# Optimization experiments

Measured on AMD Instinct MI355X. Metric: run time of the kernel, lower is better.

## Reference

```python
import jax, jax.numpy as jnp
import numpy as np

B, C, L = 4, 512, 2048
CI = 512          # inter_channels (must equal num_heads*head_dim)
H, D = 8, 64      # num_heads, head_dim = C // H
EPS = 1e-5        # BatchNorm1d eps


def setup_inputs() -> dict:
    key = jax.random.key(0)
    ks = jax.random.split(key, 9)
    s_in = 1.0 / np.sqrt(C)
    s_ci = 1.0 / np.sqrt(CI)
    return {
        "x": jax.random.normal(ks[0], (B, C, L), dtype=jnp.float32),
        "g_w": jax.random.uniform(ks[1], (CI, C), jnp.float32, -s_in, s_in),
        "g_b": jax.random.uniform(ks[2], (CI,), jnp.float32, -s_in, s_in),
        "theta_w": jax.random.uniform(ks[3], (CI, C), jnp.float32, -s_in, s_in),
        "theta_b": jax.random.uniform(ks[4], (CI,), jnp.float32, -s_in, s_in),
        "phi_w": jax.random.uniform(ks[5], (CI, C), jnp.float32, -s_in, s_in),
        "phi_b": jax.random.uniform(ks[6], (CI,), jnp.float32, -s_in, s_in),
        "w_w": jax.random.uniform(ks[7], (C, CI), jnp.float32, -s_ci, s_ci),
        "w_b": jax.random.uniform(ks[8], (C,), jnp.float32, -s_ci, s_ci),
        # BN affine params (torch inits them to 0, which zeroes the output;
        # use random values so the reference output / grads are non-trivial)
        "bn_gamma": jax.random.normal(jax.random.fold_in(key, 10), (C,), jnp.float32),
        "bn_beta": jax.random.normal(jax.random.fold_in(key, 11), (C,), jnp.float32),
    }


def _conv1x1(w, b, x):
    # x: [B, Cin, L], w: [Cout, Cin] -> [B, Cout, L]
    return jnp.einsum("oc,bcl->bol", w, x) + b[None, :, None]


def reference(x, g_w, g_b, theta_w, theta_b, phi_w, phi_b, w_w, w_b, bn_gamma, bn_beta):
    b, _, l = x.shape
    # 1x1 conv projections, split into heads: [B, H, D, L]
    g_x = _conv1x1(g_w, g_b, x).reshape(b, H, D, l).transpose(0, 1, 3, 2)      # [B,H,L,D]
    theta_x = _conv1x1(theta_w, theta_b, x).reshape(b, H, D, l).transpose(0, 1, 3, 2)  # [B,H,L,D]
    phi_x = _conv1x1(phi_w, phi_b, x).reshape(b, H, D, l)                       # [B,H,D,L]

    scale = 1.0 / jnp.sqrt(jnp.asarray(D, dtype=x.dtype))
    scores = jnp.einsum("bhqd,bhdk->bhqk", theta_x, phi_x) * scale  # [B,H,L,L]
    attn = jax.nn.softmax(scores, axis=-1)
    y = jnp.einsum("bhqk,bhkd->bhqd", attn, g_x)                    # [B,H,L,D]
    y = y.transpose(0, 1, 3, 2).reshape(b, CI, l)                   # [B,CI,L]

    # W: 1x1 conv + BatchNorm1d (training mode, biased batch stats)
    wy = _conv1x1(w_w, w_b, y)                                      # [B,C,L]
    mean = jnp.mean(wy, axis=(0, 2), keepdims=True)
    var = jnp.mean((wy - mean) ** 2, axis=(0, 2), keepdims=True)
    wy_hat = (wy - mean) * jax.lax.rsqrt(var + EPS)
    return wy_hat * bn_gamma[None, :, None] + bn_beta[None, :, None]
```

## Files before the change

kernel.cpp:

```cpp
#include <hip/hip_runtime.h>

constexpr int Bn = 4, Cn = 512, Ln = 2048, CIn = 512, Hn = 8, Dn = 64;
constexpr int COn = 3 * CIn;

typedef unsigned short u16;
typedef unsigned int u32;
typedef __attribute__((ext_vector_type(8))) short bfrag;
typedef __attribute__((ext_vector_type(4))) float facc;

#define SCF 0.180336879f

__device__ __forceinline__ facc mfma16(bfrag a, bfrag b, facc c) {
  return __builtin_amdgcn_mfma_f32_16x16x32_bf16(a, b, c, 0, 0, 0);
}

__device__ __forceinline__ void async16(const void* g, void* l) {
  __builtin_amdgcn_global_load_lds((const __attribute__((address_space(1))) void*)g,
                                   (__attribute__((address_space(3))) void*)l, 16, 0, 0);
}

__device__ __forceinline__ u16 f2bf(float x) {
  union { float f; u32 u; } v; v.f = x;
  u32 r = v.u + 0x7FFFu + ((v.u >> 16) & 1u);
  return (u16)(r >> 16);
}

__device__ __forceinline__ u16 f2bf_fast(float x) {
  union { float f; u32 u; } v; v.f = x;
  return (u16)((v.u + 0x8000u) >> 16);
}

__device__ __forceinline__ u32 pkbf(float lof, float hif) {
  union { float f; u32 u; } a, b; a.f = lof; b.f = hif;
  return __builtin_amdgcn_perm(b.u + 0x8000u, a.u + 0x8000u, 0x07060302u);
}

__device__ __forceinline__ float bflo(u32 u) { return __uint_as_float(u << 16); }
__device__ __forceinline__ float bfhi(u32 u) { return __uint_as_float(u & 0xFFFF0000u); }

__device__ __forceinline__ bfrag fr8(const u16* base, int row, int gi) {
  return *(const bfrag*)&base[row * 64 + ((gi ^ (row & 7)) * 8)];
}

__global__ void k_misc(const float* __restrict__ x, const float* __restrict__ gw,
                       const float* __restrict__ tw, const float* __restrict__ pw,
                       const float* __restrict__ ww, u16* __restrict__ xT,
                       u16* __restrict__ Wcat, u16* __restrict__ Ww,
                       float* __restrict__ stats) {
  int b = blockIdx.z;
  if (b == 4) {
    int i = (blockIdx.y * 64 + blockIdx.x) * 256 + threadIdx.x;
    if (i < CIn * Cn) {
      Wcat[i]                = f2bf(tw[i] * SCF);
      Wcat[CIn * Cn + i]     = f2bf(pw[i]);
      Wcat[2 * CIn * Cn + i] = f2bf(gw[i]);
      Ww[i]                  = f2bf(ww[i]);
    }
    if (i < 2 * Cn) stats[i] = 0.f;
    return;
  }
  __shared__ float tile[32][33];
  int l0 = blockIdx.x * 32, c0 = blockIdx.y * 32;
  int tx = threadIdx.x & 31, ty = threadIdx.x >> 5;
  const float* xb = x + (size_t)b * Cn * Ln;
  for (int k = 0; k < 4; k++)
    tile[ty + k * 8][tx] = xb[(size_t)(c0 + ty + k * 8) * Ln + l0 + tx];
  __syncthreads();
  u16* xtb = xT + (size_t)b * Ln * Cn;
  int cc = (threadIdx.x & 15) * 2, r0 = threadIdx.x >> 4;
  for (int k = 0; k < 2; k++) {
    int ll = r0 + k * 16;
    u32 pk = pkbf(tile[cc][ll], tile[cc + 1][ll]);
    *(u32*)&xtb[(size_t)(l0 + ll) * Cn + c0 + cc] = pk;
  }
}

__device__ __forceinline__ void stage128x32(const u16* g, int K, int k0, u16* lds,
                                            int w, int l) {
  int gsw = ((l & 3) ^ ((l >> 3) & 3)) * 8;
  for (int jj = 0; jj < 2; jj++) {
    int j = w * 2 + jj;
    const u16* ga = g + (size_t)(j * 16 + (l >> 2)) * K + k0 + gsw;
    async16(ga, (char*)lds + j * 1024 + l * 16);
  }
}

template <int SWAP>
__device__ __forceinline__ void gemm_core(const u16* A, const u16* Bt, int K,
                                          u16* As, u16* Bs, facc acc[4][4],
                                          int w, int l) {
  int quad = l >> 4, lo = l & 15;
  int mw = (w >> 1) * 64, nw = (w & 1) * 64;
  int rsw = (lo >> 1) & 3;
  for (int k0 = 0; k0 < K; k0 += 32) {
    stage128x32(A, K, k0, As, w, l);
    stage128x32(Bt, K, k0, Bs, w, l);
    __syncthreads();
    bfrag af[4], bfv[4];
    for (int mi = 0; mi < 4; mi++)
      af[mi] = *(const bfrag*)&As[(mw + mi * 16 + lo) * 32 + ((quad ^ rsw) * 8)];
    for (int ni = 0; ni < 4; ni++)
      bfv[ni] = *(const bfrag*)&Bs[(nw + ni * 16 + lo) * 32 + ((quad ^ rsw) * 8)];
    for (int mi = 0; mi < 4; mi++)
      for (int ni = 0; ni < 4; ni++)
        acc[mi][ni] = SWAP ? mfma16(bfv[ni], af[mi], acc[mi][ni])
                           : mfma16(af[mi], bfv[ni], acc[mi][ni]);
    __syncthreads();
  }
}

__device__ __forceinline__ void gemm_core64(const u16* A, const u16* Bt, int K,
                                            u16* As, u16* Bs, facc acc[2][4],
                                            int w, int l) {
  int quad = l >> 4, lo = l & 15;
  int mw = (w >> 1) * 32, nw = (w & 1) * 64;
  int rsw = (lo >> 1) & 3;
  int gsw = ((l & 3) ^ ((l >> 3) & 3)) * 8;
  for (int k0 = 0; k0 < K; k0 += 32) {
    async16(A + (size_t)(w * 16 + (l >> 2)) * K + k0 + gsw, (char*)As + w * 1024 + l * 16);
    stage128x32(Bt, K, k0, Bs, w, l);
    __syncthreads();
    bfrag af[2], bfv[4];
    for (int mi = 0; mi < 2; mi++)
      af[mi] = *(const bfrag*)&As[(mw + mi * 16 + lo) * 32 + ((quad ^ rsw) * 8)];
    for (int ni = 0; ni < 4; ni++)
      bfv[ni] = *(const bfrag*)&Bs[(nw + ni * 16 + lo) * 32 + ((quad ^ rsw) * 8)];
    for (int mi = 0; mi < 2; mi++)
      for (int ni = 0; ni < 4; ni++)
        acc[mi][ni] = mfma16(af[mi], bfv[ni], acc[mi][ni]);
    __syncthreads();
  }
}

__global__ __launch_bounds__(256) void k_proj(
    const u16* __restrict__ Wcat, const u16* __restrict__ xT,
    const float* __restrict__ tb, const float* __restrict__ pb,
    const float* __restrict__ gb, u16* __restrict__ Q, u16* __restrict__ Kb,
    u16* __restrict__ Vt) {
  __shared__ __align__(16) u16 As[128 * 32];
  __shared__ __align__(16) u16 Bs[128 * 32];
  int w = threadIdx.x >> 6, l = threadIdx.x & 63;
  int quad = l >> 4, lo = l & 15;
  int m0 = blockIdx.y * 128, n0 = blockIdx.x * 128, b = blockIdx.z;
  int chunk = m0 >> 9;
  facc acc[4][4] = {};
  const u16* Ap = Wcat + (size_t)m0 * Cn;
  const u16* Bp = xT + ((size_t)b * Ln + n0) * Cn;
  int mw = (w >> 1) * 64, nw = (w & 1) * 64;
  if (chunk < 2) {
    gemm_core<0>(Ap, Bp, Cn, As, Bs, acc, w, l);
    const float* bias = (chunk == 0) ? tb : pb;
    float bs = (chunk == 0) ? SCF : 1.0f;
    for (int mi = 0; mi < 4; mi++) {
      int mo = (m0 + mw + mi * 16) & 511;
      int hh = mo >> 6;
      int db = (mo & 63) + quad * 4;
      int bi = mo + quad * 4;
      u16* dst0 = ((chunk == 0) ? Q : Kb) + (size_t)(b * Hn + hh) * Ln * 64 + db;
      float b0 = bias[bi] * bs, b1 = bias[bi + 1] * bs;
      float b2 = bias[bi + 2] * bs, b3 = bias[bi + 3] * bs;
      for (int ni = 0; ni < 4; ni++) {
        int lcol = n0 + nw + ni * 16 + lo;
        facc a = acc[mi][ni];
        uint2 pk;
        pk.x = pkbf(a[0] + b0, a[1] + b1);
        pk.y = pkbf(a[2] + b2, a[3] + b3);
        *(uint2*)(dst0 + (size_t)lcol * 64) = pk;
      }
    }
  } else {
    gemm_core<1>(Ap, Bp, Cn, As, Bs, acc, w, l);
    for (int mi = 0; mi < 4; mi++) {
      int ch = (m0 + mw + mi * 16 + lo) & 511;
      int hh = ch >> 6, d = ch & 63;
      float bias = gb[ch];
      u16* dst0 = Vt + ((size_t)(b * Hn + hh) * Dn + d) * Ln;
      for (int ni = 0; ni < 4; ni++) {
        int l0 = n0 + nw + ni * 16 + quad * 4;
        facc a = acc[mi][ni];
        uint2 pk;
        pk.x = pkbf(a[0] + bias, a[1] + bias);
        pk.y = pkbf(a[2] + bias, a[3] + bias);
        *(uint2*)(dst0 + l0) = pk;
      }
    }
  }
}

__global__ __launch_bounds__(256, 2) void k_attn(
    const u16* __restrict__ Q, const u16* __restrict__ Kb,
    const u16* __restrict__ Vt, u16* __restrict__ Opart,
    float* __restrict__ lpart) {
  __shared__ __align__(16) u16 lds[24576];
  u16* Ks = lds;
  u16* Vs = lds + 8192;
  u16* QPs = lds + 16384;
  int w = threadIdx.x >> 6, l = threadIdx.x & 63;
  int quad = l >> 4, lo = l & 15;
  int q0 = blockIdx.x * 128, b = blockIdx.z;
  int h = blockIdx.y / 3, split = blockIdx.y - h * 3;
  int ts = split * 11;
  int nt = (split == 2) ? 10 : 11;
  size_t bh = (size_t)b * Hn + h;
  const u16* Qg = Q + bh * Ln * 64;
  const u16* Kg = Kb + bh * Ln * 64 + (size_t)ts * 4096;
  const u16* Vg = Vt + bh * (size_t)Dn * Ln + ts * 64;

  int rin = l >> 3;
  int gg = ((l & 7) ^ rin) * 8;

  for (int jj = 0; jj < 4; jj++) {
    int j = w * 4 + jj;
    async16(Qg + (size_t)(q0 + j * 8 + rin) * 64 + gg, (char*)QPs + j * 1024 + l * 16);
  }
  for (int jj = 0; jj < 2; jj++) {
    int j = w * 2 + jj;
    async16(Kg + (size_t)(j * 8 + rin) * 64 + gg, (char*)Ks + j * 1024 + l * 16);
    async16(Vg + (size_t)(j * 8 + rin) * Ln + gg, (char*)Vs + j * 1024 + l * 16);
  }
  __syncthreads();
  bfrag qf[2][2];
  for (int s = 0; s < 2; s++)
    for (int c = 0; c < 2; c++)
      qf[s][c] = fr8(QPs, w * 32 + s * 16 + lo, c * 4 + quad);

  facc o[2][4] = {};
  float l_i[2] = {0.f, 0.f};

  for (int t = 0; t < nt; t++) {
    const u16* Kc = Ks + (t & 1) * 4096;
    const u16* Vc = Vs + (t & 1) * 4096;
    if (t < nt - 1) {
      int nb = (~t & 1) * 4096;
      int kbase = (t + 1) * 64;
      for (int jj = 0; jj < 2; jj++) {
        int j = w * 2 + jj;
        async16(Kg + (size_t)(kbase + j * 8 + rin) * 64 + gg,
                (char*)(Ks + nb) + j * 1024 + l * 16);
        async16(Vg + (size_t)(j * 8 + rin) * Ln + kbase + gg,
                (char*)(Vs + nb) + j * 1024 + l * 16);
      }
    }
    for (int ni = 0; ni < 4; ni++) {
      bfrag kf0 = fr8(Kc, ni * 16 + lo, quad);
      bfrag kf1 = fr8(Kc, ni * 16 + lo, 4 + quad);
      for (int s = 0; s < 2; s++) {
        facc z = {};
        facc stv = mfma16(kf1, qf[s][1], mfma16(kf0, qf[s][0], z));
        float p0 = __builtin_amdgcn_exp2f(stv[0]);
        float p1 = __builtin_amdgcn_exp2f(stv[1]);
        float p2 = __builtin_amdgcn_exp2f(stv[2]);
        float p3 = __builtin_amdgcn_exp2f(stv[3]);
        l_i[s] += (p0 + p1) + (p2 + p3);
        int row = w * 32 + s * 16 + lo;
        uint2 pk;
        pk.x = pkbf(p0, p1);
        pk.y = pkbf(p2, p3);
        int gi = ni * 2 + (quad >> 1);
        *(uint2*)&QPs[row * 64 + ((gi ^ (row & 7)) * 8) + (quad & 1) * 4] = pk;
      }
    }
    bfrag pb2[2][2];
    for (int s = 0; s < 2; s++)
      for (int c = 0; c < 2; c++)
        pb2[s][c] = fr8(QPs, w * 32 + s * 16 + lo, c * 4 + quad);
    for (int mi = 0; mi < 4; mi++) {
      bfrag vf0 = fr8(Vc, mi * 16 + lo, quad);
      bfrag vf1 = fr8(Vc, mi * 16 + lo, 4 + quad);
      for (int s = 0; s < 2; s++)
        o[s][mi] = mfma16(vf1, pb2[s][1], mfma16(vf0, pb2[s][0], o[s][mi]));
    }
    __syncthreads();
  }
  int sb = split * 32 + (int)bh;
  for (int s = 0; s < 2; s++) {
    float lt = l_i[s];
    lt += __shfl_xor(lt, 16);
    lt += __shfl_xor(lt, 32);
    int q = q0 + w * 32 + s * 16 + lo;
    u16* dst = Opart + ((size_t)sb * Ln + q) * 64;
    for (int mi = 0; mi < 4; mi++) {
      uint2 pk;
      pk.x = pkbf(o[s][mi][0], o[s][mi][1]);
      pk.y = pkbf(o[s][mi][2], o[s][mi][3]);
      *(uint2*)(dst + mi * 16 + quad * 4) = pk;
    }
    if (quad == 0) lpart[(size_t)sb * Ln + q] = lt;
  }
}

__global__ void k_comb(const u16* __restrict__ Opart, const float* __restrict__ lpart,
                       u16* __restrict__ yT) {
  int i = blockIdx.x * 256 + threadIdx.x;
  int bhq = i >> 3, d0 = (i & 7) * 8;
  int bh = bhq >> 11, q = bhq & 2047;
  const u16* o1 = Opart + ((size_t)bh * Ln + q) * 64 + d0;
  const u16* o2 = o1 + (size_t)32 * Ln * 64;
  const u16* o3 = o2 + (size_t)32 * Ln * 64;
  float inv = 1.0f / (lpart[bhq] + lpart[65536 + bhq] + lpart[131072 + bhq]);
  uint4 a = *(const uint4*)o1, c = *(const uint4*)o2, e = *(const uint4*)o3;
  uint4 r;
  r.x = pkbf((bflo(a.x) + bflo(c.x) + bflo(e.x)) * inv,
             (bfhi(a.x) + bfhi(c.x) + bfhi(e.x)) * inv);
  r.y = pkbf((bflo(a.y) + bflo(c.y) + bflo(e.y)) * inv,
             (bfhi(a.y) + bfhi(c.y) + bfhi(e.y)) * inv);
  r.z = pkbf((bflo(a.z) + bflo(c.z) + bflo(e.z)) * inv,
             (bfhi(a.z) + bfhi(c.z) + bfhi(e.z)) * inv);
  r.w = pkbf((bflo(a.w) + bflo(c.w) + bflo(e.w)) * inv,
             (bfhi(a.w) + bfhi(c.w) + bfhi(e.w)) * inv);
  int b = bh >> 3, h = bh & 7;
  *(uint4*)(yT + ((size_t)b * Ln + q) * CIn + h * 64 + d0) = r;
}

__global__ __launch_bounds__(256) void k_wgemm(
    const u16* __restrict__ Ww, const u16* __restrict__ yT,
    const float* __restrict__ wb, u16* __restrict__ wy,
    float* __restrict__ stats) {
  __shared__ __align__(16) u16 As[64 * 32];
  __shared__ __align__(16) u16 Bs[128 * 32];
  int w = threadIdx.x >> 6, l = threadIdx.x & 63;
  int quad = l >> 4, lo = l & 15;
  int m0 = blockIdx.y * 64, n0 = blockIdx.x * 128, b = blockIdx.z;
  facc acc[2][4] = {};
  gemm_core64(Ww + (size_t)m0 * CIn, yT + ((size_t)b * Ln + n0) * CIn, CIn, As, Bs, acc, w, l);
  int mw = (w >> 1) * 32, nw = (w & 1) * 64;
  for (int mi = 0; mi < 2; mi++) {
    int cb = m0 + mw + mi * 16 + quad * 4;
    for (int r = 0; r < 4; r++) {
      float bias = wb[cb + r];
      float s = 0.f, q = 0.f;
      for (int ni = 0; ni < 4; ni++) {
        float v = acc[mi][ni][r] + bias;
        wy[((size_t)b * Cn + cb + r) * Ln + n0 + nw + ni * 16 + lo] = f2bf_fast(v);
        s += v; q += v * v;
      }
      for (int mask = 1; mask < 16; mask <<= 1) {
        s += __shfl_xor(s, mask);
        q += __shfl_xor(q, mask);
      }
      if (lo == 0) {
        atomicAdd(&stats[cb + r], s);
        atomicAdd(&stats[Cn + cb + r], q);
      }
    }
  }
}

__global__ void k_bn(const u16* __restrict__ wy, const float* __restrict__ stats,
                     const float* __restrict__ gam, const float* __restrict__ bet,
                     float* __restrict__ out) {
  int i = blockIdx.x * 256 + threadIdx.x;
  size_t idx = (size_t)i * 8;
  int c = (int)((idx >> 11) & (Cn - 1));
  const float invN = 1.f / (Bn * Ln);
  float mean = stats[c] * invN;
  float var = stats[Cn + c] * invN - mean * mean;
  float scl = gam[c] * rsqrtf(var + 1e-5f);
  float sh = bet[c] - mean * scl;
  uint4 v = *(const uint4*)(wy + idx);
  float4 o0, o1;
  o0.x = bflo(v.x) * scl + sh; o0.y = bfhi(v.x) * scl + sh;
  o0.z = bflo(v.y) * scl + sh; o0.w = bfhi(v.y) * scl + sh;
  o1.x = bflo(v.z) * scl + sh; o1.y = bfhi(v.z) * scl + sh;
  o1.z = bflo(v.w) * scl + sh; o1.w = bfhi(v.w) * scl + sh;
  *(float4*)(out + idx) = o0;
  *(float4*)(out + idx + 4) = o1;
}

extern "C" void kernel_launch(void* const* d_in, const int* in_sizes, int n_in,
                              void* d_out, int out_size, void* d_ws, size_t ws_size,
                              hipStream_t stream) {
  const float* x   = (const float*)d_in[0];
  const float* g_w = (const float*)d_in[1];
  const float* g_b = (const float*)d_in[2];
  const float* t_w = (const float*)d_in[3];
  const float* t_b = (const float*)d_in[4];
  const float* p_w = (const float*)d_in[5];
  const float* p_b = (const float*)d_in[6];
  const float* w_w = (const float*)d_in[7];
  const float* w_b = (const float*)d_in[8];
  const float* gam = (const float*)d_in[9];
  const float* bet = (const float*)d_in[10];
  float* out = (float*)d_out;

  char* ws = (char*)d_ws;
  size_t off = 0;
  auto alloc = [&](size_t bytes) {
    char* p = ws + off; off += (bytes + 255) & ~(size_t)255; return p;
  };
  u16*  xT   = (u16*)alloc((size_t)Bn * Ln * Cn * 2);
  u16*  Wcat = (u16*)alloc((size_t)COn * Cn * 2);
  u16*  Ww   = (u16*)alloc((size_t)Cn * CIn * 2);
  u16*  Qb   = (u16*)alloc((size_t)Bn * Hn * Ln * Dn * 2);
  u16*  Kb   = (u16*)alloc((size_t)Bn * Hn * Ln * Dn * 2);
  u16*  Vt   = (u16*)alloc((size_t)Bn * Hn * Dn * Ln * 2);
  u16*  Opart = (u16*)alloc((size_t)3 * 32 * Ln * 64 * 2);
  float* lpart = (float*)alloc((size_t)3 * 32 * Ln * 4);
  float* st  = (float*)alloc(2 * Cn * 4);
  u16* yT = Kb;
  u16* wy = Qb;
  if (ws_size < off) return;

  k_misc<<<dim3(64, 16, 5), 256, 0, stream>>>(x, g_w, t_w, p_w, w_w, xT, Wcat, Ww, st);
  k_proj<<<dim3(16, 12, 4), 256, 0, stream>>>(Wcat, xT, t_b, p_b, g_b, Qb, Kb, Vt);
  k_attn<<<dim3(16, 24, 4), 256, 0, stream>>>(Qb, Kb, Vt, Opart, lpart);
  k_comb<<<dim3(2048), 256, 0, stream>>>(Opart, lpart, yT);
  k_wgemm<<<dim3(16, 8, 4), 256, 0, stream>>>(Ww, yT, w_b, wy, st);
  k_bn<<<dim3(2048), 256, 0, stream>>>(wy, st, gam, bet, out);
}
```

Baseline: 191.3 us.

## Drop split-K attention and fuse softmax normalization into the attention epilogue

Each attention block now walks all 32 key tiles of its head instead of one third of them. It normalizes by the row sum in registers and writes the result straight into the yT layout that the output GEMM expects. This removes the separate combine kernel, the partial-output and partial-sum buffers, and the repeated Q loads across splits. In exchange the grid shrinks from 1536 blocks to 512 blocks, each with a longer serial loop. With 256 CUs at two blocks per CU that is a single wave, so any imbalance or latency can no longer be hidden by other blocks.

New measurement: 188.7 us. No clear change (-1.3%).

```diff
diff --git a/kernel.cpp b/kernel.cpp
--- a/kernel.cpp
+++ b/kernel.cpp
@@ -189,22 +189,18 @@
 
 __global__ __launch_bounds__(256, 2) void k_attn(
     const u16* __restrict__ Q, const u16* __restrict__ Kb,
-    const u16* __restrict__ Vt, u16* __restrict__ Opart,
-    float* __restrict__ lpart) {
+    const u16* __restrict__ Vt, u16* __restrict__ yT) {
   __shared__ __align__(16) u16 lds[24576];
   u16* Ks = lds;
   u16* Vs = lds + 8192;
   u16* QPs = lds + 16384;
   int w = threadIdx.x >> 6, l = threadIdx.x & 63;
   int quad = l >> 4, lo = l & 15;
-  int q0 = blockIdx.x * 128, b = blockIdx.z;
-  int h = blockIdx.y / 3, split = blockIdx.y - h * 3;
-  int ts = split * 11;
-  int nt = (split == 2) ? 10 : 11;
+  int q0 = blockIdx.x * 128, h = blockIdx.y, b = blockIdx.z;
   size_t bh = (size_t)b * Hn + h;
   const u16* Qg = Q + bh * Ln * 64;
-  const u16* Kg = Kb + bh * Ln * 64 + (size_t)ts * 4096;
-  const u16* Vg = Vt + bh * (size_t)Dn * Ln + ts * 64;
+  const u16* Kg = Kb + bh * Ln * 64;
+  const u16* Vg = Vt + bh * (size_t)Dn * Ln;
 
   int rin = l >> 3;
   int gg = ((l & 7) ^ rin) * 8;
@@ -227,10 +223,10 @@
   facc o[2][4] = {};
   float l_i[2] = {0.f, 0.f};
 
-  for (int t = 0; t < nt; t++) {
+  for (int t = 0; t < 32; t++) {
     const u16* Kc = Ks + (t & 1) * 4096;
     const u16* Vc = Vs + (t & 1) * 4096;
-    if (t < nt - 1) {
+    if (t < 31) {
       int nb = (~t & 1) * 4096;
       int kbase = (t + 1) * 64;
       for (int jj = 0; jj < 2; jj++) {
@@ -272,44 +268,20 @@
     }
     __syncthreads();
   }
-  int sb = split * 32 + (int)bh;
   for (int s = 0; s < 2; s++) {
     float lt = l_i[s];
     lt += __shfl_xor(lt, 16);
     lt += __shfl_xor(lt, 32);
+    float inv = 1.0f / lt;
     int q = q0 + w * 32 + s * 16 + lo;
-    u16* dst = Opart + ((size_t)sb * Ln + q) * 64;
+    u16* dst = yT + ((size_t)b * Ln + q) * CIn + h * 64;
     for (int mi = 0; mi < 4; mi++) {
       uint2 pk;
-      pk.x = pkbf(o[s][mi][0], o[s][mi][1]);
-      pk.y = pkbf(o[s][mi][2], o[s][mi][3]);
+      pk.x = pkbf(o[s][mi][0] * inv, o[s][mi][1] * inv);
+      pk.y = pkbf(o[s][mi][2] * inv, o[s][mi][3] * inv);
       *(uint2*)(dst + mi * 16 + quad * 4) = pk;
     }
-    if (quad == 0) lpart[(size_t)sb * Ln + q] = lt;
-  }
-}
-
-__global__ void k_comb(const u16* __restrict__ Opart, const float* __restrict__ lpart,
-                       u16* __restrict__ yT) {
-  int i = blockIdx.x * 256 + threadIdx.x;
-  int bhq = i >> 3, d0 = (i & 7) * 8;
-  int bh = bhq >> 11, q = bhq & 2047;
-  const u16* o1 = Opart + ((size_t)bh * Ln + q) * 64 + d0;
-  const u16* o2 = o1 + (size_t)32 * Ln * 64;
-  const u16* o3 = o2 + (size_t)32 * Ln * 64;
-  float inv = 1.0f / (lpart[bhq] + lpart[65536 + bhq] + lpart[131072 + bhq]);
-  uint4 a = *(const uint4*)o1, c = *(const uint4*)o2, e = *(const uint4*)o3;
-  uint4 r;
-  r.x = pkbf((bflo(a.x) + bflo(c.x) + bflo(e.x)) * inv,
-             (bfhi(a.x) + bfhi(c.x) + bfhi(e.x)) * inv);
-  r.y = pkbf((bflo(a.y) + bflo(c.y) + bflo(e.y)) * inv,
-             (bfhi(a.y) + bfhi(c.y) + bfhi(e.y)) * inv);
-  r.z = pkbf((bflo(a.z) + bflo(c.z) + bflo(e.z)) * inv,
-             (bfhi(a.z) + bfhi(c.z) + bfhi(e.z)) * inv);
-  r.w = pkbf((bflo(a.w) + bflo(c.w) + bflo(e.w)) * inv,
-             (bfhi(a.w) + bfhi(c.w) + bfhi(e.w)) * inv);
-  int b = bh >> 3, h = bh & 7;
-  *(uint4*)(yT + ((size_t)b * Ln + q) * CIn + h * 64 + d0) = r;
+  }
 }
 
 __global__ __launch_bounds__(256) void k_wgemm(
@@ -394,17 +366,14 @@
   u16*  Qb   = (u16*)alloc((size_t)Bn * Hn * Ln * Dn * 2);
   u16*  Kb   = (u16*)alloc((size_t)Bn * Hn * Ln * Dn * 2);
   u16*  Vt   = (u16*)alloc((size_t)Bn * Hn * Dn * Ln * 2);
-  u16*  Opart = (u16*)alloc((size_t)3 * 32 * Ln * 64 * 2);
-  float* lpart = (float*)alloc((size_t)3 * 32 * Ln * 4);
+  u16*  yT   = (u16*)alloc((size_t)Bn * Ln * CIn * 2);
+  u16*  wy   = (u16*)alloc((size_t)Bn * Cn * Ln * 2);
   float* st  = (float*)alloc(2 * Cn * 4);
-  u16* yT = Kb;
-  u16* wy = Qb;
   if (ws_size < off) return;
 
   k_misc<<<dim3(64, 16, 5), 256, 0, stream>>>(x, g_w, t_w, p_w, w_w, xT, Wcat, Ww, st);
   k_proj<<<dim3(16, 12, 4), 256, 0, stream>>>(Wcat, xT, t_b, p_b, g_b, Qb, Kb, Vt);
-  k_attn<<<dim3(16, 24, 4), 256, 0, stream>>>(Qb, Kb, Vt, Opart, lpart);
-  k_comb<<<dim3(2048), 256, 0, stream>>>(Opart, lpart, yT);
+  k_attn<<<dim3(16, 8, 4), 256, 0, stream>>>(Qb, Kb, Vt, yT);
   k_wgemm<<<dim3(16, 8, 4), 256, 0, stream>>>(Ww, yT, w_b, wy, st);
   k_bn<<<dim3(2048), 256, 0, stream>>>(wy, st, gam, bet, out);
 }
```
